# Performance work log

Hardware: AMD Instinct MI355X
Metric: run time of the kernel (lower is better)

Reference implementation:

```python
import jax, jax.numpy as jnp
import numpy as np

HEADS = 16
DIM_HEAD = 64
QUERY_DIM = 1024
INNER = HEADS * DIM_HEAD  # 1024
SCALE = DIM_HEAD ** -0.5
B, T = 4, 2048


def setup_inputs() -> dict:
    key = jax.random.key(0)
    ks = jax.random.split(key, 7)
    s = 0.02
    return {
        "hidden_states": jax.random.normal(ks[0], (B, T, QUERY_DIM), dtype=jnp.float32),
        "attention_mask": jax.random.randint(ks[1], (B, T), 0, 2, dtype=jnp.int32),
        "Wq": jax.random.normal(ks[2], (QUERY_DIM, INNER), dtype=jnp.float32) * s,
        "Wk": jax.random.normal(ks[3], (QUERY_DIM, INNER), dtype=jnp.float32) * s,
        "Wv": jax.random.normal(ks[4], (QUERY_DIM, INNER), dtype=jnp.float32) * s,
        "Wo": jax.random.normal(ks[5], (INNER, QUERY_DIM), dtype=jnp.float32) * s,
        "bo": jnp.zeros((QUERY_DIM,), dtype=jnp.float32),
    }


def reference(hidden_states, attention_mask, Wq, Wk, Wv, Wo, bo):
    # QKV projections (bias=False)
    q = hidden_states @ Wq  # [B,T,INNER]
    k = hidden_states @ Wk
    v = hidden_states @ Wv
    # split heads: b t (h d) -> b h t d
    def split(x):
        b, t, _ = x.shape
        return x.reshape(b, t, HEADS, DIM_HEAD).transpose(0, 2, 1, 3)
    q, k, v = split(q), split(k), split(v)
    sim = jnp.einsum('bhid,bhjd->bhij', q, k) * SCALE  # [B,H,T,T]
    neg = jnp.finfo(sim.dtype).min
    mask = attention_mask[:, None, None, :]  # [B,1,1,T]
    sim = jnp.where(mask == 0, neg, sim)
    attn = jax.nn.softmax(sim, axis=-1)
    out = jnp.einsum('bhij,bhjd->bhid', attn, v)  # [B,H,T,D]
    out = out.transpose(0, 2, 1, 3).reshape(hidden_states.shape[0], hidden_states.shape[1], INNER)
    return out @ Wo + bo  # dropout p=0.0 -> identity
```

## Files before the change

### kernel.cpp

```cpp
#include <hip/hip_runtime.h>
#include <stdint.h>

typedef __attribute__((ext_vector_type(8))) __bf16 bf16x8;
typedef __attribute__((ext_vector_type(4))) float f32x4;
typedef __attribute__((ext_vector_type(16))) float f32x16;
typedef __attribute__((ext_vector_type(4))) unsigned u32x4;

#define QSCALE 0.18033688011112042f

static __device__ __forceinline__ unsigned short f2bf(float x) {
  return __builtin_bit_cast(unsigned short, (__bf16)x);
}
static __device__ __forceinline__ unsigned pkbf(float a, float b) {
  union { unsigned short h[2]; unsigned u; } r;
  r.h[0] = f2bf(a); r.h[1] = f2bf(b); return r.u;
}
static __device__ __forceinline__ void async16(const void* g, void* l) {
  __builtin_amdgcn_global_load_lds(
      (const __attribute__((address_space(1))) void*)g,
      (__attribute__((address_space(3))) void*)l, 16, 0, 0);
}

__global__ __launch_bounds__(256) void k_prep(const float* __restrict__ hs,
                                              const float* __restrict__ Wq,
                                              const float* __restrict__ Wk,
                                              const float* __restrict__ Wv,
                                              const float* __restrict__ Wo,
                                              const int* __restrict__ mask,
                                              unsigned short* __restrict__ hs_bf,
                                              unsigned short* __restrict__ wt_qkv,
                                              unsigned short* __restrict__ wot,
                                              float* __restrict__ bias_all) {
  __shared__ float tile[64][65];
  const int bid = blockIdx.x;
  if (bid < 8192) {
    const int i = bid * 256 + threadIdx.x;
    float4 v = ((const float4*)hs)[i];
    ushort4 o;
    o.x = f2bf(v.x); o.y = f2bf(v.y); o.z = f2bf(v.z); o.w = f2bf(v.w);
    ((ushort4*)hs_bf)[i] = o;
    return;
  }
  if (bid >= 9216) {
    const int b = bid - 9216;
#pragma unroll
    for (int j = 0; j < 8; ++j) {
      const int t = j * 256 + threadIdx.x;
      bias_all[b * 2048 + t] = (mask[b * 2048 + t] == 0) ? -__builtin_inff() : 0.0f;
    }
    return;
  }
  const int idx = bid - 8192;
  const int mat = idx >> 8;
  const float* W = (mat == 0) ? Wq : (mat == 1) ? Wk : (mat == 2) ? Wv : Wo;
  const float scale = (mat == 0) ? QSCALE : 1.0f;
  const int n0 = (idx & 15) * 64, k0 = ((idx >> 4) & 15) * 64;
  const int t = threadIdx.x, c = t & 63;
#pragma unroll
  for (int j = 0; j < 16; ++j) {
    int r = j * 4 + (t >> 6);
    tile[r][c] = W[(size_t)(k0 + r) * 1024 + n0 + c] * scale;
  }
  __syncthreads();
  unsigned short* dst = (mat < 3) ? (wt_qkv + (size_t)mat * 1024 * 1024) : wot;
#pragma unroll
  for (int j = 0; j < 16; ++j) {
    int nr = j * 4 + (t >> 6);
    dst[(size_t)(n0 + nr) * 1024 + k0 + c] = f2bf(tile[c][nr]);
  }
}

__global__ __launch_bounds__(256) void k_gemm_qkv(const unsigned short* __restrict__ A,
                                                  const unsigned short* __restrict__ Bt,
                                                  unsigned short* __restrict__ q_lin,
                                                  unsigned short* __restrict__ k_lin,
                                                  unsigned short* __restrict__ vT) {
  __shared__ __align__(16) unsigned short aT[2][128 * 32];
  __shared__ __align__(16) unsigned short bT[2][128 * 32];
  const int tid = threadIdx.x, lane = tid & 63, w = tid >> 6;
  const int wr = w >> 1, wc = w & 1;
  int flat = blockIdx.y * 24 + blockIdx.x;
  flat = (flat & 7) * 192 + (flat >> 3);
  const int m0 = (flat / 24) * 128, n0 = (flat % 24) * 128;
  const char* Ab = (const char*)A;
  const char* Bb = (const char*)Bt;
  char* aTb = (char*)aT; char* bTb = (char*)bT;
  f32x4 acc[4][4] = {};

  const int ci0 = w * 2, bo0 = ci0 * 1024 + lane * 16;
  const int srow0 = bo0 >> 6, scol0 = bo0 & 63;
#define G_STAGE(buf, kt)                                                              \
  {                                                                                   \
    _Pragma("unroll")                                                                 \
    for (int j = 0; j < 2; ++j) {                                                     \
      const int row = srow0 + j * 16;                                                 \
      async16(Ab + ((size_t)(m0 + row) * 1024 + (kt) * 32) * 2 + scol0,               \
              aTb + (buf) * 8192 + (ci0 + j) * 1024);                                 \
      async16(Bb + ((size_t)(n0 + row) * 1024 + (kt) * 32) * 2 + scol0,               \
              bTb + (buf) * 8192 + (ci0 + j) * 1024);                                 \
    }                                                                                 \
  }

  G_STAGE(0, 0);
  __syncthreads();
  for (int kt = 0; kt < 32; ++kt) {
    const int cur = kt & 1;
    if (kt + 1 < 32) G_STAGE(cur ^ 1, kt + 1);
    bf16x8 af[4], bfr[4];
#pragma unroll
    for (int mi = 0; mi < 4; ++mi)
      af[mi] = *(const bf16x8*)(aTb + cur * 8192 +
               ((wr * 64 + mi * 16 + (lane & 15)) * 32 + (lane >> 4) * 8) * 2);
#pragma unroll
    for (int ni = 0; ni < 4; ++ni)
      bfr[ni] = *(const bf16x8*)(bTb + cur * 8192 +
               ((wc * 64 + ni * 16 + (lane & 15)) * 32 + (lane >> 4) * 8) * 2);
#pragma unroll
    for (int mi = 0; mi < 4; ++mi)
#pragma unroll
      for (int ni = 0; ni < 4; ++ni)
        acc[mi][ni] = __builtin_amdgcn_mfma_f32_16x16x32_bf16(af[mi], bfr[ni], acc[mi][ni], 0, 0, 0);
    __syncthreads();
  }
#undef G_STAGE

  const int mat = n0 >> 10;
  const int nn0 = n0 & 1023;
  if (mat < 2) {
    unsigned short* dst = (mat == 0) ? q_lin : k_lin;
#pragma unroll
    for (int mi = 0; mi < 4; ++mi) {
      const int r0 = m0 + wr * 64 + mi * 16 + (lane >> 4) * 4;
#pragma unroll
      for (int ni = 0; ni < 4; ++ni) {
        const int c = nn0 + wc * 64 + ni * 16 + (lane & 15);
#pragma unroll
        for (int r = 0; r < 4; ++r)
          dst[(size_t)(r0 + r) * 1024 + c] = f2bf(acc[mi][ni][r]);
      }
    }
  } else {
#pragma unroll
    for (int mi = 0; mi < 4; ++mi) {
      const int r0 = m0 + wr * 64 + mi * 16 + (lane >> 4) * 4;
      const int b = r0 >> 11, tt = r0 & 2047;
#pragma unroll
      for (int ni = 0; ni < 4; ++ni) {
        const int c = nn0 + wc * 64 + ni * 16 + (lane & 15);
        const int h = c >> 6, d = c & 63;
        ushort4 o;
        o.x = f2bf(acc[mi][ni][0]); o.y = f2bf(acc[mi][ni][1]);
        o.z = f2bf(acc[mi][ni][2]); o.w = f2bf(acc[mi][ni][3]);
        *(ushort4*)(vT + ((size_t)((b * 16 + h) * 64 + d) << 11) + tt) = o;
      }
    }
  }
}

__global__ __launch_bounds__(256, 4) void k_attn(const unsigned short* __restrict__ q_lin,
                                                 const unsigned short* __restrict__ k_lin,
                                                 const unsigned short* __restrict__ vT,
                                                 const float* __restrict__ bias_all,
                                                 unsigned short* __restrict__ o_lin) {
  __shared__ __align__(16) unsigned short Kt[2][64 * 64];
  __shared__ __align__(16) unsigned short Vt[2][64 * 64];
  __shared__ __align__(16) float biasl[2][64];
  const int tid = threadIdx.x, lane = tid & 63, w = tid >> 6;
  const int qi = lane & 31, hi = lane >> 5;
  int flat = blockIdx.y * 16 + blockIdx.x;
  flat = (flat & 7) * 128 + (flat >> 3);
  const int bh = flat >> 4, b = bh >> 4, h = bh & 15;
  const int t0 = (flat & 15) * 128;
  const unsigned short* qbp = q_lin + (size_t)b * 2048 * 1024 + h * 64;
  const unsigned short* kbp = k_lin + (size_t)b * 2048 * 1024 + h * 64;
  const unsigned short* vbp = vT + ((size_t)bh * 64 << 11);
  unsigned short* obp = o_lin + (size_t)b * 2048 * 1024 + h * 64;
  const char* bbp = (const char*)(bias_all + b * 2048);
  char* KtB = (char*)Kt; char* VtB = (char*)Vt;
  char* blB = (char*)biasl;
  const int rsw = (qi & 7) << 4;

  bf16x8 qf[4];
  {
    const unsigned short* qrow = qbp + (size_t)(t0 + w * 32 + qi) * 1024;
#pragma unroll
    for (int s = 0; s < 4; ++s)
      qf[s] = *(const bf16x8*)(qrow + s * 16 + hi * 8);
  }

  f32x16 oaccA = {}, oaccB = {};
  float m_ = -3.0e38f, l_ = 0.f;

  const int sci = w * 2, sbo = sci * 1024 + lane * 16;
  const int srow = sbo >> 7;
  const int scolb = (sbo & 127) ^ ((srow & 7) << 4);
#define A_STAGE(buf, kv0)                                                             \
  {                                                                                   \
    _Pragma("unroll")                                                                 \
    for (int j = 0; j < 2; ++j) {                                                     \
      const int row = srow + j * 8;                                                   \
      async16(kbp + (size_t)((kv0) + row) * 1024 + (scolb >> 1),                      \
              KtB + (buf) * 8192 + (sci + j) * 1024);                                 \
      async16(vbp + (size_t)row * 2048 + (kv0) + (scolb >> 1),                        \
              VtB + (buf) * 8192 + (sci + j) * 1024);                                 \
    }                                                                                 \
    if (lane < 16) async16(bbp + (size_t)(kv0) * 4 + lane * 16,                       \
                           blB + (buf) * 256 + lane * 16);                            \
  }

  A_STAGE(0, 0);
  __syncthreads();

  for (int kt = 0; kt < 32; ++kt) {
    const int cur = kt & 1;
    if (kt + 1 < 32) A_STAGE(cur ^ 1, (kt + 1) * 64);

    f32x16 sA = {}, sB = {};
    __builtin_amdgcn_s_setprio(1);
#pragma unroll
    for (int s = 0; s < 4; ++s) {
      bf16x8 kf = *(const bf16x8*)(KtB + cur * 8192 + (qi)*128 + ((s * 32 + hi * 16) ^ rsw));
      sA = __builtin_amdgcn_mfma_f32_32x32x16_bf16(kf, qf[s], sA, 0, 0, 0);
    }
#pragma unroll
    for (int s = 0; s < 4; ++s) {
      bf16x8 kf = *(const bf16x8*)(KtB + cur * 8192 + (32 + qi) * 128 + ((s * 32 + hi * 16) ^ rsw));
      sB = __builtin_amdgcn_mfma_f32_32x32x16_bf16(kf, qf[s], sB, 0, 0, 0);
    }
    __builtin_amdgcn_s_setprio(0);

    float e[32];
#pragma unroll
    for (int u = 0; u < 4; ++u) {
      const float4 b4 = ((const float4*)biasl[cur])[2 * u + hi];
      e[4 * u + 0] = sA[4 * u + 0] + b4.x; e[4 * u + 1] = sA[4 * u + 1] + b4.y;
      e[4 * u + 2] = sA[4 * u + 2] + b4.z; e[4 * u + 3] = sA[4 * u + 3] + b4.w;
    }
#pragma unroll
    for (int u = 0; u < 4; ++u) {
      const float4 b4 = ((const float4*)biasl[cur])[8 + 2 * u + hi];
      e[16 + 4 * u + 0] = sB[4 * u + 0] + b4.x; e[16 + 4 * u + 1] = sB[4 * u + 1] + b4.y;
      e[16 + 4 * u + 2] = sB[4 * u + 2] + b4.z; e[16 + 4 * u + 3] = sB[4 * u + 3] + b4.w;
    }

    float t16[16];
#pragma unroll
    for (int i = 0; i < 16; ++i) t16[i] = fmaxf(e[i], e[16 + i]);
#pragma unroll
    for (int i = 0; i < 8; ++i) t16[i] = fmaxf(t16[i], t16[8 + i]);
#pragma unroll
    for (int i = 0; i < 4; ++i) t16[i] = fmaxf(t16[i], t16[4 + i]);
    float mt = fmaxf(fmaxf(t16[0], t16[1]), fmaxf(t16[2], t16[3]));
    mt = fmaxf(mt, __shfl_xor(mt, 32));

    if (__any(mt > m_ + 8.0f)) {
      const float mn = fmaxf(m_, mt);
      const float sf = __builtin_amdgcn_exp2f(m_ - mn);
      m_ = mn; l_ *= sf;
#pragma unroll
      for (int r = 0; r < 16; ++r) { oaccA[r] *= sf; oaccB[r] *= sf; }
    }

#pragma unroll
    for (int i = 0; i < 32; ++i) e[i] = __builtin_amdgcn_exp2f(e[i] - m_);
    float u16[16];
#pragma unroll
    for (int i = 0; i < 16; ++i) u16[i] = e[i] + e[16 + i];
#pragma unroll
    for (int i = 0; i < 8; ++i) u16[i] += u16[8 + i];
#pragma unroll
    for (int i = 0; i < 4; ++i) u16[i] += u16[4 + i];
    float rs = (u16[0] + u16[1]) + (u16[2] + u16[3]);
    l_ += rs + __shfl_xor(rs, 32);

    unsigned d[16];
#pragma unroll
    for (int j = 0; j < 8; ++j) {
      d[2 * j] = pkbf(e[4 * j + 0], e[4 * j + 1]);
      d[2 * j + 1] = pkbf(e[4 * j + 2], e[4 * j + 3]);
    }
    unsigned rcv[8];
#pragma unroll
    for (int t = 0; t < 4; ++t)
#pragma unroll
      for (int s = 0; s < 2; ++s) {
        const unsigned snd = hi ? d[4 * t + s] : d[4 * t + 2 + s];
        rcv[2 * t + s] = __shfl_xor(snd, 32);
      }
    bf16x8 pw[4];
#pragma unroll
    for (int t = 0; t < 4; ++t) {
      u32x4 u4;
      u4.x = hi ? rcv[2 * t + 0] : d[4 * t + 0];
      u4.y = hi ? rcv[2 * t + 1] : d[4 * t + 1];
      u4.z = hi ? d[4 * t + 2] : rcv[2 * t + 0];
      u4.w = hi ? d[4 * t + 3] : rcv[2 * t + 1];
      pw[t] = __builtin_bit_cast(bf16x8, u4);
    }

    __builtin_amdgcn_s_setprio(1);
#pragma unroll
    for (int t = 0; t < 4; ++t) {
      bf16x8 vf = *(const bf16x8*)(VtB + cur * 8192 + (qi)*128 + ((t * 32 + hi * 16) ^ rsw));
      oaccA = __builtin_amdgcn_mfma_f32_32x32x16_bf16(vf, pw[t], oaccA, 0, 0, 0);
    }
#pragma unroll
    for (int t = 0; t < 4; ++t) {
      bf16x8 vf = *(const bf16x8*)(VtB + cur * 8192 + (32 + qi) * 128 + ((t * 32 + hi * 16) ^ rsw));
      oaccB = __builtin_amdgcn_mfma_f32_32x32x16_bf16(vf, pw[t], oaccB, 0, 0, 0);
    }
    __builtin_amdgcn_s_setprio(0);
    __syncthreads();
  }
#undef A_STAGE

  const float inv = 1.0f / l_;
  unsigned short* orow = obp + (size_t)(t0 + w * 32 + qi) * 1024;
#pragma unroll
  for (int u = 0; u < 4; ++u) {
    ushort4 oa, ob;
    oa.x = f2bf(oaccA[4 * u + 0] * inv); oa.y = f2bf(oaccA[4 * u + 1] * inv);
    oa.z = f2bf(oaccA[4 * u + 2] * inv); oa.w = f2bf(oaccA[4 * u + 3] * inv);
    ob.x = f2bf(oaccB[4 * u + 0] * inv); ob.y = f2bf(oaccB[4 * u + 1] * inv);
    ob.z = f2bf(oaccB[4 * u + 2] * inv); ob.w = f2bf(oaccB[4 * u + 3] * inv);
    *(ushort4*)(orow + 8 * u + 4 * hi) = oa;
    *(ushort4*)(orow + 32 + 8 * u + 4 * hi) = ob;
  }
}

__global__ __launch_bounds__(256) void k_gemm_out(const unsigned short* __restrict__ A,
                                                  const unsigned short* __restrict__ Bt,
                                                  const float* __restrict__ bias,
                                                  float* __restrict__ out) {
  __shared__ __align__(16) unsigned short aT[2][128 * 32];
  __shared__ __align__(16) unsigned short bT[2][128 * 32];
  const int tid = threadIdx.x, lane = tid & 63, w = tid >> 6;
  const int wr = w >> 1, wc = w & 1;
  int flat = blockIdx.y * 8 + blockIdx.x;
  flat = (flat & 7) * 64 + (flat >> 3);
  const int m0 = (flat >> 3) * 128, n0 = (flat & 7) * 128;
  const char* Ab = (const char*)A;
  const char* Bb = (const char*)Bt;
  char* aTb = (char*)aT; char* bTb = (char*)bT;
  f32x4 acc[4][4] = {};

  const int ci0 = w * 2, bo0 = ci0 * 1024 + lane * 16;
  const int srow0 = bo0 >> 6, scol0 = bo0 & 63;
#define G_STAGE(buf, kt)                                                              \
  {                                                                                   \
    _Pragma("unroll")                                                                 \
    for (int j = 0; j < 2; ++j) {                                                     \
      const int row = srow0 + j * 16;                                                 \
      async16(Ab + ((size_t)(m0 + row) * 1024 + (kt) * 32) * 2 + scol0,               \
              aTb + (buf) * 8192 + (ci0 + j) * 1024);                                 \
      async16(Bb + ((size_t)(n0 + row) * 1024 + (kt) * 32) * 2 + scol0,               \
              bTb + (buf) * 8192 + (ci0 + j) * 1024);                                 \
    }                                                                                 \
  }

  G_STAGE(0, 0);
  __syncthreads();
  for (int kt = 0; kt < 32; ++kt) {
    const int cur = kt & 1;
    if (kt + 1 < 32) G_STAGE(cur ^ 1, kt + 1);
    bf16x8 af[4], bfr[4];
#pragma unroll
    for (int mi = 0; mi < 4; ++mi)
      af[mi] = *(const bf16x8*)(aTb + cur * 8192 +
               ((wr * 64 + mi * 16 + (lane & 15)) * 32 + (lane >> 4) * 8) * 2);
#pragma unroll
    for (int ni = 0; ni < 4; ++ni)
      bfr[ni] = *(const bf16x8*)(bTb + cur * 8192 +
               ((wc * 64 + ni * 16 + (lane & 15)) * 32 + (lane >> 4) * 8) * 2);
#pragma unroll
    for (int mi = 0; mi < 4; ++mi)
#pragma unroll
      for (int ni = 0; ni < 4; ++ni)
        acc[mi][ni] = __builtin_amdgcn_mfma_f32_16x16x32_bf16(af[mi], bfr[ni], acc[mi][ni], 0, 0, 0);
    __syncthreads();
  }
#undef G_STAGE
#pragma unroll
  for (int mi = 0; mi < 4; ++mi) {
    const int r0 = m0 + wr * 64 + mi * 16 + (lane >> 4) * 4;
#pragma unroll
    for (int ni = 0; ni < 4; ++ni) {
      const int c = n0 + wc * 64 + ni * 16 + (lane & 15);
      const float bb = bias[c];
#pragma unroll
      for (int r = 0; r < 4; ++r)
        out[(size_t)(r0 + r) * 1024 + c] = acc[mi][ni][r] + bb;
    }
  }
}

extern "C" void kernel_launch(void* const* d_in, const int* in_sizes, int n_in,
                              void* d_out, int out_size, void* d_ws, size_t ws_size,
                              hipStream_t stream) {
  const float* hs   = (const float*)d_in[0];
  const int*   mask = (const int*)d_in[1];
  const float* Wq   = (const float*)d_in[2];
  const float* Wk   = (const float*)d_in[3];
  const float* Wv   = (const float*)d_in[4];
  const float* Wo   = (const float*)d_in[5];
  const float* bo   = (const float*)d_in[6];
  float* out = (float*)d_out;

  const size_t MB = 1024 * 1024;
  char* ws = (char*)d_ws;
  unsigned short* hs_bf  = (unsigned short*)(ws);
  unsigned short* wt_qkv = (unsigned short*)(ws + 16 * MB);
  unsigned short* wot    = (unsigned short*)(ws + 22 * MB);
  unsigned short* q_lin  = (unsigned short*)(ws + 24 * MB);
  unsigned short* k_lin  = (unsigned short*)(ws + 40 * MB);
  unsigned short* vT     = (unsigned short*)(ws + 56 * MB);
  unsigned short* o_lin  = (unsigned short*)(ws + 72 * MB);
  float*          bias_a = (float*)(ws + 88 * MB);

  k_prep<<<9220, 256, 0, stream>>>(hs, Wq, Wk, Wv, Wo, mask, hs_bf, wt_qkv, wot, bias_a);
  k_gemm_qkv<<<dim3(24, 64), 256, 0, stream>>>(hs_bf, wt_qkv, q_lin, k_lin, vT);
  k_attn<<<dim3(16, 64), 256, 0, stream>>>(q_lin, k_lin, vT, bias_a, o_lin);
  k_gemm_out<<<dim3(8, 64), 256, 0, stream>>>(o_lin, wot, bo, out);
}
```

Measured before the change: 312.2 us.

## Store Q/K/V in MFMA-fragment-friendly grouped layout and drop P shuffle

The QKV GEMM epilogue now writes Q, K and V in a per-head layout grouped into 8-element d- or t-chunks, with K rows permuted so the attention kernel's score fragments line up directly with the PV MFMA operand. The attention kernel stages contiguous 16-byte chunks with no XOR swizzle, reads conflict-free LDS fragments, and builds the P operand by packing without cross-lane shuffles. The cost is scattered 2-byte stores in the QKV epilogue for Q and K, and a permuted bias lookup to match the reordered key positions.

```diff
diff --git a/kernel.cpp b/kernel.cpp
--- a/kernel.cpp
+++ b/kernel.cpp
@@ -19,6 +19,9 @@
   __builtin_amdgcn_global_load_lds(
       (const __attribute__((address_space(1))) void*)g,
       (__attribute__((address_space(3))) void*)l, 16, 0, 0);
+}
+static __device__ __forceinline__ int bsw23(int t) {
+  return (t & ~12) | ((t & 4) << 1) | ((t & 8) >> 1);
 }
 
 __global__ __launch_bounds__(256) void k_prep(const float* __restrict__ hs,
@@ -72,9 +75,9 @@
 
 __global__ __launch_bounds__(256) void k_gemm_qkv(const unsigned short* __restrict__ A,
                                                   const unsigned short* __restrict__ Bt,
-                                                  unsigned short* __restrict__ q_lin,
-                                                  unsigned short* __restrict__ k_lin,
-                                                  unsigned short* __restrict__ vT) {
+                                                  unsigned short* __restrict__ qG,
+                                                  unsigned short* __restrict__ kG,
+                                                  unsigned short* __restrict__ vG) {
   __shared__ __align__(16) unsigned short aT[2][128 * 32];
   __shared__ __align__(16) unsigned short bT[2][128 * 32];
   const int tid = threadIdx.x, lane = tid & 63, w = tid >> 6;
@@ -127,23 +130,28 @@
   const int mat = n0 >> 10;
   const int nn0 = n0 & 1023;
   if (mat < 2) {
-    unsigned short* dst = (mat == 0) ? q_lin : k_lin;
-#pragma unroll
-    for (int mi = 0; mi < 4; ++mi) {
-      const int r0 = m0 + wr * 64 + mi * 16 + (lane >> 4) * 4;
-#pragma unroll
-      for (int ni = 0; ni < 4; ++ni) {
-        const int c = nn0 + wc * 64 + ni * 16 + (lane & 15);
-#pragma unroll
-        for (int r = 0; r < 4; ++r)
-          dst[(size_t)(r0 + r) * 1024 + c] = f2bf(acc[mi][ni][r]);
-      }
-    }
-  } else {
+    unsigned short* dst = (mat == 0) ? qG : kG;
 #pragma unroll
     for (int mi = 0; mi < 4; ++mi) {
       const int r0 = m0 + wr * 64 + mi * 16 + (lane >> 4) * 4;
       const int b = r0 >> 11, tt = r0 & 2047;
+      const int pt = (mat == 0) ? tt : bsw23(tt);
+#pragma unroll
+      for (int ni = 0; ni < 4; ++ni) {
+        const int c = nn0 + wc * 64 + ni * 16 + (lane & 15);
+        const int h = c >> 6, d = c & 63, g = d >> 3, dm = d & 7;
+        const size_t base = (((size_t)(b * 16 + h) * 8 + g) * 2048 + pt) * 8 + dm;
+#pragma unroll
+        for (int r = 0; r < 4; ++r)
+          dst[base + (size_t)r * 8] = f2bf(acc[mi][ni][r]);
+      }
+    }
+  } else {
+#pragma unroll
+    for (int mi = 0; mi < 4; ++mi) {
+      const int r0 = m0 + wr * 64 + mi * 16 + (lane >> 4) * 4;
+      const int b = r0 >> 11, tt = r0 & 2047;
+      const int tg = tt >> 3, tm = tt & 7;
 #pragma unroll
       for (int ni = 0; ni < 4; ++ni) {
         const int c = nn0 + wc * 64 + ni * 16 + (lane & 15);
@@ -151,19 +159,19 @@
         ushort4 o;
         o.x = f2bf(acc[mi][ni][0]); o.y = f2bf(acc[mi][ni][1]);
         o.z = f2bf(acc[mi][ni][2]); o.w = f2bf(acc[mi][ni][3]);
-        *(ushort4*)(vT + ((size_t)((b * 16 + h) * 64 + d) << 11) + tt) = o;
+        *(ushort4*)(vG + ((((size_t)(b * 16 + h) * 256 + tg) * 64 + d) * 8 + tm)) = o;
       }
     }
   }
 }
 
-__global__ __launch_bounds__(256, 4) void k_attn(const unsigned short* __restrict__ q_lin,
-                                                 const unsigned short* __restrict__ k_lin,
-                                                 const unsigned short* __restrict__ vT,
+__global__ __launch_bounds__(256, 4) void k_attn(const unsigned short* __restrict__ qG,
+                                                 const unsigned short* __restrict__ kG,
+                                                 const unsigned short* __restrict__ vG,
                                                  const float* __restrict__ bias_all,
                                                  unsigned short* __restrict__ o_lin) {
-  __shared__ __align__(16) unsigned short Kt[2][64 * 64];
-  __shared__ __align__(16) unsigned short Vt[2][64 * 64];
+  __shared__ __align__(16) unsigned short Kt[2][4096];
+  __shared__ __align__(16) unsigned short Vt[2][4096];
   __shared__ __align__(16) float biasl[2][64];
   const int tid = threadIdx.x, lane = tid & 63, w = tid >> 6;
   const int qi = lane & 31, hi = lane >> 5;
@@ -171,38 +179,33 @@
   flat = (flat & 7) * 128 + (flat >> 3);
   const int bh = flat >> 4, b = bh >> 4, h = bh & 15;
   const int t0 = (flat & 15) * 128;
-  const unsigned short* qbp = q_lin + (size_t)b * 2048 * 1024 + h * 64;
-  const unsigned short* kbp = k_lin + (size_t)b * 2048 * 1024 + h * 64;
-  const unsigned short* vbp = vT + ((size_t)bh * 64 << 11);
+  const char* qGb = (const char*)(qG + (size_t)bh * 131072);
+  const char* kGb = (const char*)(kG + (size_t)bh * 131072);
+  const char* vGb = (const char*)(vG + (size_t)bh * 131072);
   unsigned short* obp = o_lin + (size_t)b * 2048 * 1024 + h * 64;
   const char* bbp = (const char*)(bias_all + b * 2048);
   char* KtB = (char*)Kt; char* VtB = (char*)Vt;
   char* blB = (char*)biasl;
-  const int rsw = (qi & 7) << 4;
-
+
+  const int qrow = t0 + w * 32 + qi;
   bf16x8 qf[4];
-  {
-    const unsigned short* qrow = qbp + (size_t)(t0 + w * 32 + qi) * 1024;
-#pragma unroll
-    for (int s = 0; s < 4; ++s)
-      qf[s] = *(const bf16x8*)(qrow + s * 16 + hi * 8);
-  }
+#pragma unroll
+  for (int s = 0; s < 4; ++s)
+    qf[s] = *(const bf16x8*)(qGb + ((size_t)((2 * s + hi) * 2048 + qrow)) * 16);
 
   f32x16 oaccA = {}, oaccB = {};
   float m_ = -3.0e38f, l_ = 0.f;
 
-  const int sci = w * 2, sbo = sci * 1024 + lane * 16;
-  const int srow = sbo >> 7;
-  const int scolb = (sbo & 127) ^ ((srow & 7) << 4);
+  const int g0 = w * 2;
 #define A_STAGE(buf, kv0)                                                             \
   {                                                                                   \
     _Pragma("unroll")                                                                 \
     for (int j = 0; j < 2; ++j) {                                                     \
-      const int row = srow + j * 8;                                                   \
-      async16(kbp + (size_t)((kv0) + row) * 1024 + (scolb >> 1),                      \
-              KtB + (buf) * 8192 + (sci + j) * 1024);                                 \
-      async16(vbp + (size_t)row * 2048 + (kv0) + (scolb >> 1),                        \
-              VtB + (buf) * 8192 + (sci + j) * 1024);                                 \
+      const int g = g0 + j;                                                           \
+      async16(kGb + ((size_t)(g * 2048 + (kv0) + lane)) * 16,                         \
+              KtB + (buf) * 8192 + g * 1024);                                         \
+      async16(vGb + ((size_t)((kv0) * 8 + g * 64 + lane)) * 16,                       \
+              VtB + (buf) * 8192 + g * 1024);                                         \
     }                                                                                 \
     if (lane < 16) async16(bbp + (size_t)(kv0) * 4 + lane * 16,                       \
                            blB + (buf) * 256 + lane * 16);                            \
@@ -211,20 +214,22 @@
   A_STAGE(0, 0);
   __syncthreads();
 
+#pragma unroll 2
   for (int kt = 0; kt < 32; ++kt) {
     const int cur = kt & 1;
     if (kt + 1 < 32) A_STAGE(cur ^ 1, (kt + 1) * 64);
 
+    const char* Kb = KtB + cur * 8192 + qi * 16 + hi * 1024;
     f32x16 sA = {}, sB = {};
     __builtin_amdgcn_s_setprio(1);
 #pragma unroll
     for (int s = 0; s < 4; ++s) {
-      bf16x8 kf = *(const bf16x8*)(KtB + cur * 8192 + (qi)*128 + ((s * 32 + hi * 16) ^ rsw));
+      bf16x8 kf = *(const bf16x8*)(Kb + s * 2048);
       sA = __builtin_amdgcn_mfma_f32_32x32x16_bf16(kf, qf[s], sA, 0, 0, 0);
     }
 #pragma unroll
     for (int s = 0; s < 4; ++s) {
-      bf16x8 kf = *(const bf16x8*)(KtB + cur * 8192 + (32 + qi) * 128 + ((s * 32 + hi * 16) ^ rsw));
+      bf16x8 kf = *(const bf16x8*)(Kb + s * 2048 + 512);
       sB = __builtin_amdgcn_mfma_f32_32x32x16_bf16(kf, qf[s], sB, 0, 0, 0);
     }
     __builtin_amdgcn_s_setprio(0);
@@ -232,15 +237,13 @@
     float e[32];
 #pragma unroll
     for (int u = 0; u < 4; ++u) {
-      const float4 b4 = ((const float4*)biasl[cur])[2 * u + hi];
+      const int f4 = ((u & 2) << 1) + (u & 1) + (hi << 1);
+      const float4 b4 = ((const float4*)(blB + cur * 256))[f4];
       e[4 * u + 0] = sA[4 * u + 0] + b4.x; e[4 * u + 1] = sA[4 * u + 1] + b4.y;
       e[4 * u + 2] = sA[4 * u + 2] + b4.z; e[4 * u + 3] = sA[4 * u + 3] + b4.w;
-    }
-#pragma unroll
-    for (int u = 0; u < 4; ++u) {
-      const float4 b4 = ((const float4*)biasl[cur])[8 + 2 * u + hi];
-      e[16 + 4 * u + 0] = sB[4 * u + 0] + b4.x; e[16 + 4 * u + 1] = sB[4 * u + 1] + b4.y;
-      e[16 + 4 * u + 2] = sB[4 * u + 2] + b4.z; e[16 + 4 * u + 3] = sB[4 * u + 3] + b4.w;
+      const float4 c4 = ((const float4*)(blB + cur * 256))[f4 + 8];
+      e[16 + 4 * u + 0] = sB[4 * u + 0] + c4.x; e[16 + 4 * u + 1] = sB[4 * u + 1] + c4.y;
+      e[16 + 4 * u + 2] = sB[4 * u + 2] + c4.z; e[16 + 4 * u + 3] = sB[4 * u + 3] + c4.w;
     }
 
     float t16[16];
@@ -273,40 +276,27 @@
     float rs = (u16[0] + u16[1]) + (u16[2] + u16[3]);
     l_ += rs + __shfl_xor(rs, 32);
 
-    unsigned d[16];
-#pragma unroll
-    for (int j = 0; j < 8; ++j) {
-      d[2 * j] = pkbf(e[4 * j + 0], e[4 * j + 1]);
-      d[2 * j + 1] = pkbf(e[4 * j + 2], e[4 * j + 3]);
-    }
-    unsigned rcv[8];
-#pragma unroll
-    for (int t = 0; t < 4; ++t)
-#pragma unroll
-      for (int s = 0; s < 2; ++s) {
-        const unsigned snd = hi ? d[4 * t + s] : d[4 * t + 2 + s];
-        rcv[2 * t + s] = __shfl_xor(snd, 32);
-      }
     bf16x8 pw[4];
 #pragma unroll
     for (int t = 0; t < 4; ++t) {
       u32x4 u4;
-      u4.x = hi ? rcv[2 * t + 0] : d[4 * t + 0];
-      u4.y = hi ? rcv[2 * t + 1] : d[4 * t + 1];
-      u4.z = hi ? d[4 * t + 2] : rcv[2 * t + 0];
-      u4.w = hi ? d[4 * t + 3] : rcv[2 * t + 1];
+      u4.x = pkbf(e[8 * t + 0], e[8 * t + 1]);
+      u4.y = pkbf(e[8 * t + 2], e[8 * t + 3]);
+      u4.z = pkbf(e[8 * t + 4], e[8 * t + 5]);
+      u4.w = pkbf(e[8 * t + 6], e[8 * t + 7]);
       pw[t] = __builtin_bit_cast(bf16x8, u4);
     }
 
+    const char* Vb = VtB + cur * 8192 + qi * 16 + hi * 1024;
     __builtin_amdgcn_s_setprio(1);
 #pragma unroll
     for (int t = 0; t < 4; ++t) {
-      bf16x8 vf = *(const bf16x8*)(VtB + cur * 8192 + (qi)*128 + ((t * 32 + hi * 16) ^ rsw));
+      bf16x8 vf = *(const bf16x8*)(Vb + t * 2048);
       oaccA = __builtin_amdgcn_mfma_f32_32x32x16_bf16(vf, pw[t], oaccA, 0, 0, 0);
     }
 #pragma unroll
     for (int t = 0; t < 4; ++t) {
-      bf16x8 vf = *(const bf16x8*)(VtB + cur * 8192 + (32 + qi) * 128 + ((t * 32 + hi * 16) ^ rsw));
+      bf16x8 vf = *(const bf16x8*)(Vb + t * 2048 + 512);
       oaccB = __builtin_amdgcn_mfma_f32_32x32x16_bf16(vf, pw[t], oaccB, 0, 0, 0);
     }
     __builtin_amdgcn_s_setprio(0);
@@ -315,7 +305,7 @@
 #undef A_STAGE
 
   const float inv = 1.0f / l_;
-  unsigned short* orow = obp + (size_t)(t0 + w * 32 + qi) * 1024;
+  unsigned short* orow = obp + (size_t)qrow * 1024;
 #pragma unroll
   for (int u = 0; u < 4; ++u) {
     ushort4 oa, ob;
@@ -411,14 +401,14 @@
   unsigned short* hs_bf  = (unsigned short*)(ws);
   unsigned short* wt_qkv = (unsigned short*)(ws + 16 * MB);
   unsigned short* wot    = (unsigned short*)(ws + 22 * MB);
-  unsigned short* q_lin  = (unsigned short*)(ws + 24 * MB);
-  unsigned short* k_lin  = (unsigned short*)(ws + 40 * MB);
-  unsigned short* vT     = (unsigned short*)(ws + 56 * MB);
+  unsigned short* qG     = (unsigned short*)(ws + 24 * MB);
+  unsigned short* kG     = (unsigned short*)(ws + 40 * MB);
+  unsigned short* vG     = (unsigned short*)(ws + 56 * MB);
   unsigned short* o_lin  = (unsigned short*)(ws + 72 * MB);
   float*          bias_a = (float*)(ws + 88 * MB);
 
   k_prep<<<9220, 256, 0, stream>>>(hs, Wq, Wk, Wv, Wo, mask, hs_bf, wt_qkv, wot, bias_a);
-  k_gemm_qkv<<<dim3(24, 64), 256, 0, stream>>>(hs_bf, wt_qkv, q_lin, k_lin, vT);
-  k_attn<<<dim3(16, 64), 256, 0, stream>>>(q_lin, k_lin, vT, bias_a, o_lin);
+  k_gemm_qkv<<<dim3(24, 64), 256, 0, stream>>>(hs_bf, wt_qkv, qG, kG, vG);
+  k_attn<<<dim3(16, 64), 256, 0, stream>>>(qG, kG, vG, bias_a, o_lin);
   k_gemm_out<<<dim3(8, 64), 256, 0, stream>>>(o_lin, wot, bo, out);
 }
```

Measured after the change: 301.4 us. 3.4% less time.
